# Kernel tuning notes

Measured on AMD Instinct MI355X. Metric: run time of the kernel, lower is better.

Reference implementation:

```python
import jax, jax.numpy as jnp
import numpy as np

B, NPG, DEG = 512, 128, 16          # graphs, nodes/graph, out-degree
N = B * NPG                          # 65536 nodes
E = N * DEG                          # 1048576 edges
IN_DIM, HID, HEADS = 11, 32, 4
K1 = int(np.ceil(0.8 * NPG))         # 103 nodes/graph after pool1
K2 = int(np.ceil(0.8 * K1))          # 83 nodes/graph after pool2


def gat_conv(x, src, dst, mask, W, a_s, a_d, b, n_nodes):
    # PyG GATConv (concat=True, add_self_loops=True, eval mode -> no dropout)
    xp = (x @ W).reshape(n_nodes, HEADS, HID)            # [N,H,C]
    as_ = jnp.einsum('nhc,hc->nh', xp, a_s)
    ad_ = jnp.einsum('nhc,hc->nh', xp, a_d)
    loop = jnp.arange(n_nodes)
    s = jnp.concatenate([src, loop])
    d = jnp.concatenate([dst, loop])
    m = jnp.concatenate([mask, jnp.ones(n_nodes, bool)])
    logit = jax.nn.leaky_relu(as_[s] + ad_[d], 0.2)      # [E+N,H]
    logit = jnp.where(m[:, None], logit, -1e9)
    mx = jax.ops.segment_max(logit, d, num_segments=n_nodes)
    ex = jnp.exp(logit - mx[d]) * m[:, None]
    den = jax.ops.segment_sum(ex, d, num_segments=n_nodes)
    alpha = ex / (den[d] + 1e-16)                        # segment softmax over dst
    out = jax.ops.segment_sum(alpha[:, :, None] * xp[s], d, num_segments=n_nodes)
    return out.reshape(n_nodes, HEADS * HID) + b


def topk_pool(x, src, dst, mask, w, npg, k):
    # PyG TopKPooling: score = tanh((x*w).sum(-1)/||w||); keep top ceil(ratio*n) per graph
    nb = x.shape[0] // npg
    score = jnp.tanh((x @ w) / jnp.linalg.norm(w))
    vals, idx = jax.lax.top_k(score.reshape(nb, npg), k)  # [B,k]
    perm = (idx + (jnp.arange(nb) * npg)[:, None]).reshape(-1)
    x_new = x[perm] * vals.reshape(-1, 1)
    remap = jnp.full(nb * npg, -1).at[perm].set(jnp.arange(nb * k))
    ns, nd = remap[src], remap[dst]
    m = mask & (ns >= 0) & (nd >= 0)
    return x_new, jnp.where(m, ns, 0), jnp.where(m, nd, 0), m


def setup_inputs():
    key = jax.random.key(0)
    ks = jax.random.split(key, 24)
    s = 0.05
    x = jax.random.normal(ks[0], (N, IN_DIM), jnp.float32)
    src = jnp.repeat(jnp.arange(N), DEG)
    dst = (src // NPG) * NPG + jax.random.randint(ks[1], (E,), 0, NPG)
    edge_index = jnp.stack([src, dst])
    edge_attr = jax.random.normal(ks[2], (E, 4), jnp.float32)
    batch = jnp.repeat(jnp.arange(B), NPG)
    p = dict(
        W_g1=jax.random.normal(ks[3], (IN_DIM, HEADS * HID), jnp.float32) * s,
        att_src1=jax.random.normal(ks[4], (HEADS, HID), jnp.float32) * s,
        att_dst1=jax.random.normal(ks[5], (HEADS, HID), jnp.float32) * s,
        b_g1=jnp.zeros((HEADS * HID,), jnp.float32),
        W_t1=jax.random.normal(ks[6], (HEADS * HID, HID), jnp.float32) * s,
        b_t1=jnp.zeros((HID,), jnp.float32),
        pool_w1=jax.random.normal(ks[7], (HID,), jnp.float32) * s,
        W_g2=jax.random.normal(ks[8], (HID, HEADS * HID), jnp.float32) * s,
        att_src2=jax.random.normal(ks[9], (HEADS, HID), jnp.float32) * s,
        att_dst2=jax.random.normal(ks[10], (HEADS, HID), jnp.float32) * s,
        b_g2=jnp.zeros((HEADS * HID,), jnp.float32),
        W_t2=jax.random.normal(ks[11], (HEADS * HID, HID), jnp.float32) * s,
        b_t2=jnp.zeros((HID,), jnp.float32),
        pool_w2=jax.random.normal(ks[12], (HID,), jnp.float32) * s,
        W_l1=jax.random.normal(ks[13], (2 * HID, 256), jnp.float32) * s,
        b_l1=jnp.zeros((256,), jnp.float32),
        W_l2=jax.random.normal(ks[14], (256, 1024), jnp.float32) * s,
        b_l2=jnp.zeros((1024,), jnp.float32),
        W_l3=jax.random.normal(ks[15], (1024, 1), jnp.float32) * s,
        b_l3=jnp.zeros((1,), jnp.float32),
    )
    return dict(x=x, edge_index=edge_index, edge_attr=edge_attr, batch=batch, **p)


def reference(x, edge_index, edge_attr, batch,
              W_g1, att_src1, att_dst1, b_g1, W_t1, b_t1, pool_w1,
              W_g2, att_src2, att_dst2, b_g2, W_t2, b_t2, pool_w2,
              W_l1, b_l1, W_l2, b_l2, W_l3, b_l3):
    # edge_attr is ignored (GATConv built without edge_dim); batch is implicit
    # in the fixed equal-size graph layout.  Eval mode -> dropout disabled.
    src, dst = edge_index[0], edge_index[1]
    mask = jnp.ones(E, bool)
    h = jax.nn.relu(gat_conv(x, src, dst, mask, W_g1, att_src1, att_dst1, b_g1, N))
    h = h @ W_t1 + b_t1
    h, src, dst, mask = topk_pool(h, src, dst, mask, pool_w1, NPG, K1)
    h1 = h.reshape(B, K1, HID)
    g1 = jnp.concatenate([h1.max(1), h1.mean(1)], axis=1)   # [B, 2*HID]
    h = jax.nn.relu(gat_conv(h, src, dst, mask, W_g2, att_src2, att_dst2, b_g2, B * K1))
    h = h @ W_t2 + b_t2
    h, src, dst, mask = topk_pool(h, src, dst, mask, pool_w2, K1, K2)
    h2 = h.reshape(B, K2, HID)
    g2 = jnp.concatenate([h2.max(1), h2.mean(1)], axis=1)
    g = g1 + g2
    g = jax.nn.relu(g @ W_l1 + b_l1)
    g = jax.nn.relu(g @ W_l2 + b_l2)
    return g @ W_l3 + b_l3                                   # [B,1]
```

## Files before the change

kernel.cpp:

```cpp
#include <hip/hip_runtime.h>
#include <math.h>

constexpr int NPGc  = 128;
constexpr int NG    = 512;
constexpr int EPGc  = 2048;
constexpr int ETOT  = 1048576;
constexpr int IND   = 11;
constexpr int HIDc  = 32;
constexpr int FD    = 128;
constexpr int K1c   = 103;
constexpr int K2c   = 83;
constexpr int NN    = NG * NPGc;
constexpr int N2c   = NG * K1c;

__device__ __forceinline__ float lrelu(float x){ return fmaxf(x, 0.2f*x); }

__device__ __forceinline__ unsigned flipF(float f){
    unsigned u = __float_as_uint(f);
    return u ^ (unsigned)(((int)u >> 31) | 0x80000000);
}
__device__ __forceinline__ float unflipF(unsigned u){
    unsigned m = ((u >> 31) - 1u) | 0x80000000u;
    return __uint_as_float(u ^ m);
}

template<int KIN>
__device__ void foldDev(const float* __restrict__ Wg, const float* __restrict__ avs,
                        const float* __restrict__ avd, float* __restrict__ S, float* __restrict__ D, int t)
{
    if (t < KIN * 4) {
        int k = t >> 2, h = t & 3;
        float s = 0.f, d = 0.f;
        for (int j = 0; j < HIDc; j++) {
            float w = Wg[k*FD + h*HIDc + j];
            s = fmaf(w, avs[h*HIDc + j], s);
            d = fmaf(w, avd[h*HIDc + j], d);
        }
        S[t] = s; D[t] = d;
    }
}

__global__ __launch_bounds__(256) void k_prep(const int* __restrict__ ei,
    const float* __restrict__ W1g, const float* __restrict__ s1, const float* __restrict__ d1,
    const float* __restrict__ W2g, const float* __restrict__ s2, const float* __restrict__ d2,
    int* __restrict__ csrOff, unsigned char* __restrict__ csrSB, unsigned char* __restrict__ csrDB,
    float* __restrict__ S1, float* __restrict__ D1, float* __restrict__ S2, float* __restrict__ D2)
{
    int b = blockIdx.x, t = threadIdx.x;
    if (b >= NG) {
        if (b == NG)     foldDev<IND>(W1g, s1, d1, S1, D1, t);
        else             foldDev<HIDc>(W2g, s2, d2, S2, D2, t);
        return;
    }
    int g = b;
    __shared__ int cnt[128], cur[128], offL[129];
    __shared__ unsigned char sbL[EPGc], dbL[EPGc];
    if (t < 128) cnt[t] = 0;
    __syncthreads();
    const int* dstG = ei + ETOT + g * EPGc;
    int dnv[8];
    #pragma unroll
    for (int q = 0; q < 8; q++) {
        int e = t + 256*q;
        dnv[q] = dstG[e] - g * NPGc;
        atomicAdd(&cnt[dnv[q]], 1);
    }
    __syncthreads();
    if (t < 64) {
        int c0 = cnt[2*t], c1 = cnt[2*t + 1], ps = c0 + c1, P = ps;
        #pragma unroll
        for (int dl = 1; dl < 64; dl <<= 1) { int v = __shfl_up(P, dl); if (t >= dl) P += v; }
        int E0 = P - ps;
        offL[2*t] = E0; offL[2*t + 1] = E0 + c0;
        cur[2*t]  = E0; cur[2*t + 1]  = E0 + c0;
        if (t == 63) offL[128] = P;
    }
    __syncthreads();
    #pragma unroll
    for (int q = 0; q < 8; q++) {
        int e = t + 256*q;
        int pos = atomicAdd(&cur[dnv[q]], 1);
        sbL[pos] = (unsigned char)(e >> 4);
        dbL[pos] = (unsigned char)dnv[q];
    }
    __syncthreads();
    if (t < 128) {
        ((int4*)(csrSB + (size_t)g * EPGc))[t] = ((const int4*)sbL)[t];
        ((int4*)(csrDB + (size_t)g * EPGc))[t] = ((const int4*)dbL)[t];
    }
    if (t <= NPGc) csrOff[g*132 + t] = offL[t];
}

template<int NNODE, int KIN, int KEEP, bool FIRST>
__global__ __launch_bounds__(256, 4) void k_layer(
    const float* __restrict__ xin, const float* __restrict__ Wg,
    const float* __restrict__ WsS, const float* __restrict__ WsD,
    const float* __restrict__ bg,
    const float* __restrict__ Wt, const float* __restrict__ bt,
    const float* __restrict__ pw,
    const int* __restrict__ csrOff, const unsigned char* __restrict__ csrSB,
    const unsigned char* __restrict__ csrDB,
    const int* __restrict__ ei,
    int* __restrict__ csrOffW, unsigned char* __restrict__ sbW,
    unsigned char* __restrict__ dbW,
    float* __restrict__ xnew,
    float* __restrict__ gfeat, const float* __restrict__ gprev,
    const float* __restrict__ W1, const float* __restrict__ b1,
    const float* __restrict__ W2, const float* __restrict__ b2,
    const float* __restrict__ W3, const float* __restrict__ b3,
    float* __restrict__ outp)
{
    constexpr int NP   = (NNODE + 3) & ~3;
    constexpr int NGRP = NP / 4;
    int g = blockIdx.x, t = threadIdx.x;

    __shared__ __align__(16) float xFT[KIN * NP];
    __shared__ __align__(16) float WgsL[KIN * 32];
    __shared__ __align__(16) float WtsL[1024];
    __shared__ __align__(16) float xpL[NP * 36];
    __shared__ float wEu[EPGc];
    __shared__ unsigned char sbL[EPGc], dbL[EPGc];
    __shared__ int offL[NNODE + 1 > 129 ? NNODE + 1 : 129];
    __shared__ float asL[NNODE], adL[NNODE], sfW[NNODE], sDi[NNODE];
    __shared__ unsigned maxU[NNODE];
    __shared__ float WsSL[KIN * 4], WsDL[KIN * 4], bgL[FD], btL[HIDc];
    __shared__ float gvec[64];
    float* mLn = (float*)maxU;

    {
        const float* xg = xin + (size_t)g * NNODE * KIN;
        for (int i = t; i < NNODE * KIN; i += 256) {
            int n = i / KIN, k = i - n * KIN;
            xFT[k * NP + n] = xg[i];
        }
        if constexpr (NP > NNODE) {
            for (int i = t; i < KIN * (NP - NNODE); i += 256) {
                int k = i / (NP - NNODE), n = NNODE + (i % (NP - NNODE));
                xFT[k * NP + n] = 0.f;
            }
        }
    }
    for (int i = t; i < KIN * 4; i += 256) { WsSL[i] = WsS[i]; WsDL[i] = WsD[i]; }
    if (t < FD) bgL[t] = bg[t];
    if (t < HIDc) btL[t] = bt[t];
    if (t <= NNODE) offL[t] = csrOff[g*132 + t];
    for (int i = t; i < EPGc / 16; i += 256) {
        ((int4*)sbL)[i] = ((const int4*)(csrSB + (size_t)g * EPGc))[i];
        ((int4*)dbL)[i] = ((const int4*)(csrDB + (size_t)g * EPGc))[i];
    }
    __syncthreads();
    const int EC = offL[NNODE];

    const int n4 = t >> 3, j4 = t & 7;
    float4 acc0, acc1, acc2, acc3;
    { float4 bi = make_float4(btL[j4*4], btL[j4*4+1], btL[j4*4+2], btL[j4*4+3]);
      acc0 = bi; acc1 = bi; acc2 = bi; acc3 = bi; }

    for (int h = 0; h < 4; h++) {
        __syncthreads();

        for (int i = t; i < KIN * 32; i += 256) WgsL[i] = Wg[(i >> 5)*FD + h*32 + (i & 31)];
        ((float4*)WtsL)[t] = ((const float4*)(Wt + h*1024))[t];
        __syncthreads();

        for (int id = t; id < NGRP * 32; id += 256) {
            int grp = id >> 5, c = id & 31;
            float4 a = make_float4(0.f, 0.f, 0.f, 0.f);
            #pragma unroll
            for (int k = 0; k < KIN; k++) {
                float4 xv = *(const float4*)&xFT[k * NP + grp * 4];
                float w = WgsL[k*32 + c];
                a.x = fmaf(xv.x, w, a.x); a.y = fmaf(xv.y, w, a.y);
                a.z = fmaf(xv.z, w, a.z); a.w = fmaf(xv.w, w, a.w);
            }
            int nb = grp * 4;
            xpL[(nb+0)*36 + c] = a.x; xpL[(nb+1)*36 + c] = a.y;
            xpL[(nb+2)*36 + c] = a.z; xpL[(nb+3)*36 + c] = a.w;
        }
        if (t < NNODE) {
            float s = 0.f, d = 0.f;
            #pragma unroll
            for (int k = 0; k < KIN; k++) {
                float v = xFT[k * NP + t];
                s = fmaf(v, WsSL[k*4 + h], s);
                d = fmaf(v, WsDL[k*4 + h], d);
            }
            asL[t] = s; adL[t] = d; maxU[t] = flipF(s);
        }
        __syncthreads();

        for (int s = t; s < EC; s += 256)
            atomicMax(&maxU[dbL[s]], flipF(asL[sbL[s]]));
        __syncthreads();

        if (t < NNODE) {
            float ad = adL[t];
            float m = lrelu(unflipF(maxU[t]) + ad);
            sfW[t] = expf(lrelu(asL[t] + ad) - m);
            mLn[t] = m;
        }
        __syncthreads();

        for (int s = t; s < EC; s += 256) {
            int sb = sbL[s], db = dbL[s];
            wEu[s] = expf(lrelu(asL[sb] + adL[db]) - mLn[db]);
        }
        __syncthreads();

        if (t < NNODE) {
            float den = sfW[t];
            int lo = offL[t], hi = offL[t + 1];
            for (int s = lo; s < hi; s++) den += wEu[s];
            sDi[t] = 1.f / (den + 1e-16f);
        }
        __syncthreads();

        const float4* X4 = (const float4*)xpL;
        auto aggOne = [&](int p) -> float4 {
            int n = p >> 3, c4 = p & 7;
            float w0 = sfW[n];
            float4 v = X4[n*9 + c4];
            float4 a; a.x = w0*v.x; a.y = w0*v.y; a.z = w0*v.z; a.w = w0*v.w;
            int lo = offL[n], hi = offL[n + 1];
            for (int s = lo; s < hi; s++) {
                int sc = sbL[s]; float w = wEu[s];
                float4 u = X4[sc*9 + c4];
                a.x = fmaf(w, u.x, a.x); a.y = fmaf(w, u.y, a.y);
                a.z = fmaf(w, u.z, a.z); a.w = fmaf(w, u.w, a.w);
            }
            float inv = sDi[n];
            float4 r;
            r.x = fmaxf(fmaf(a.x, inv, bgL[h*32 + c4*4 + 0]), 0.f);
            r.y = fmaxf(fmaf(a.y, inv, bgL[h*32 + c4*4 + 1]), 0.f);
            r.z = fmaxf(fmaf(a.z, inv, bgL[h*32 + c4*4 + 2]), 0.f);
            r.w = fmaxf(fmaf(a.w, inv, bgL[h*32 + c4*4 + 3]), 0.f);
            return r;
        };
        float4 rv0 = aggOne(t);
        float4 rv1 = aggOne(t + 256);
        float4 rv2 = aggOne(t + 512);
        float4 rv3;
        if (t + 768 < NNODE * 8) rv3 = aggOne(t + 768);
        __syncthreads();

        float4* X4w = (float4*)xpL;
        X4w[(t>>3)*9 + (t&7)] = rv0;
        { int p = t + 256; X4w[(p>>3)*9 + (p&7)] = rv1; }
        { int p = t + 512; X4w[(p>>3)*9 + (p&7)] = rv2; }
        if (t + 768 < NNODE * 8) { int p = t + 768; X4w[(p>>3)*9 + (p&7)] = rv3; }
        __syncthreads();

        if (n4 < NGRP) {
            int nb = n4 * 4;
            #pragma unroll 8
            for (int c = 0; c < 32; c++) {
                float4 w4 = *(const float4*)&WtsL[c*HIDc + j4*4];
                float r0 = xpL[(nb+0)*36 + c], r1 = xpL[(nb+1)*36 + c];
                float r2 = xpL[(nb+2)*36 + c], r3 = xpL[(nb+3)*36 + c];
                acc0.x = fmaf(r0, w4.x, acc0.x); acc0.y = fmaf(r0, w4.y, acc0.y);
                acc0.z = fmaf(r0, w4.z, acc0.z); acc0.w = fmaf(r0, w4.w, acc0.w);
                acc1.x = fmaf(r1, w4.x, acc1.x); acc1.y = fmaf(r1, w4.y, acc1.y);
                acc1.z = fmaf(r1, w4.z, acc1.z); acc1.w = fmaf(r1, w4.w, acc1.w);
                acc2.x = fmaf(r2, w4.x, acc2.x); acc2.y = fmaf(r2, w4.y, acc2.y);
                acc2.z = fmaf(r2, w4.z, acc2.z); acc2.w = fmaf(r2, w4.w, acc2.w);
                acc3.x = fmaf(r3, w4.x, acc3.x); acc3.y = fmaf(r3, w4.y, acc3.y);
                acc3.z = fmaf(r3, w4.z, acc3.z); acc3.w = fmaf(r3, w4.w, acc3.w);
            }
        }
    }
    __syncthreads();

    float* htL = xpL;
    if (n4 < NGRP) {
        int nb = n4 * 4, jb = j4 * 4;
        float4 av[4] = {acc0, acc1, acc2, acc3};
        #pragma unroll
        for (int i = 0; i < 4; i++) {
            int n = nb + i;
            if (n < NNODE) {
                htL[n*33 + jb + 0] = av[i].x; htL[n*33 + jb + 1] = av[i].y;
                htL[n*33 + jb + 2] = av[i].z; htL[n*33 + jb + 3] = av[i].w;
            }
        }
    }
    __syncthreads();

    float* scoreL = wEu;
    int*   rnkL   = (int*)(wEu + 128);
    float nrm; { float ss = 0.f; for (int k = 0; k < HIDc; k++) { float w = pw[k]; ss = fmaf(w, w, ss); } nrm = sqrtf(ss); }
    if (t < NNODE) {
        float dot = 0.f;
        for (int k = 0; k < HIDc; k++) dot = fmaf(htL[t*33 + k], pw[k], dot);
        scoreL[t] = tanhf(dot / nrm);
    }
    __syncthreads();
    if (t < NNODE) {
        float si = scoreL[t]; int rank = 0;
        for (int q = 0; q < NNODE; q++) {
            float sj = scoreL[q];
            rank += (sj > si || (sj == si && q < t)) ? 1 : 0;
        }
        rnkL[t] = (rank < KEEP) ? rank : -1;
    }
    __syncthreads();
    if constexpr (FIRST) {
        for (int p = t; p < NNODE * 32; p += 256) {
            int n = p >> 5, jj = p & 31;
            int rk = rnkL[n];
            if (rk >= 0) xnew[((size_t)g*KEEP + rk)*HIDc + jj] = htL[n*33 + jj] * scoreL[n];
        }
    }
    if (t < HIDc) {
        float mx = -INFINITY, sm = 0.f;
        for (int n = 0; n < NNODE; n++) {
            if (rnkL[n] >= 0) { float v = htL[n*33 + t] * scoreL[n]; mx = fmaxf(mx, v); sm += v; }
        }
        float mean = sm / (float)KEEP;
        if constexpr (FIRST) {
            gfeat[(size_t)g*64 + t]      = mx;
            gfeat[(size_t)g*64 + 32 + t] = mean;
        } else {
            gvec[t]      = gprev[(size_t)g*64 + t] + mx;
            gvec[32 + t] = gprev[(size_t)g*64 + 32 + t] + mean;
        }
    }

    if constexpr (FIRST) {
        __syncthreads();
        int* cnt = (int*)maxU;
        int* cur = (int*)sfW;
        if (t < 128) cnt[t] = 0;
        __syncthreads();
        const int* dstG = ei + ETOT + g * EPGc;
        int snv[8], dnv[8];
        #pragma unroll
        for (int q = 0; q < 8; q++) {
            int e = t + 256*q;
            int s = rnkL[e >> 4], d = rnkL[dstG[e] - g * NPGc];
            bool ok = (s >= 0 && d >= 0);
            snv[q] = s; dnv[q] = ok ? d : -1;
            if (ok) atomicAdd(&cnt[d], 1);
        }
        __syncthreads();
        if (t < 64) {
            int c0 = cnt[2*t], c1 = cnt[2*t + 1], ps = c0 + c1, P = ps;
            #pragma unroll
            for (int dl = 1; dl < 64; dl <<= 1) { int v = __shfl_up(P, dl); if (t >= dl) P += v; }
            int E0 = P - ps;
            offL[2*t] = E0; offL[2*t + 1] = E0 + c0;
            cur[2*t]  = E0; cur[2*t + 1]  = E0 + c0;
            if (t == 63) offL[128] = P;
        }
        __syncthreads();
        #pragma unroll
        for (int q = 0; q < 8; q++) {
            if (dnv[q] >= 0) {
                int pos = atomicAdd(&cur[dnv[q]], 1);
                sbL[pos] = (unsigned char)snv[q];
                dbL[pos] = (unsigned char)dnv[q];
            }
        }
        __syncthreads();
        if (t < 128) {
            ((int4*)(sbW + (size_t)g * EPGc))[t] = ((const int4*)sbL)[t];
            ((int4*)(dbW + (size_t)g * EPGc))[t] = ((const int4*)dbL)[t];
        }
        if (t <= K1c) csrOffW[g*132 + t] = offL[t];
    } else {
        __syncthreads();
        float* h1L = wEu;
        float* red = wEu + 256;
        float a = b1[t];
        #pragma unroll 4
        for (int k = 0; k < 64; k++) a = fmaf(gvec[k], W1[k*256 + t], a);
        h1L[t] = fmaxf(a, 0.f);
        __syncthreads();
        float c0 = b2[t], c1 = b2[t + 256], c2 = b2[t + 512], c3 = b2[t + 768];
        const float* w2c = W2 + t;
        #pragma unroll 4
        for (int i = 0; i < 256; i++) {
            float hv = h1L[i];
            const float* wr = w2c + (size_t)i * 1024;
            c0 = fmaf(hv, wr[0],   c0);
            c1 = fmaf(hv, wr[256], c1);
            c2 = fmaf(hv, wr[512], c2);
            c3 = fmaf(hv, wr[768], c3);
        }
        float p = fmaf(fmaxf(c0, 0.f), W3[t],
                  fmaf(fmaxf(c1, 0.f), W3[t + 256],
                  fmaf(fmaxf(c2, 0.f), W3[t + 512],
                       fmaxf(c3, 0.f) * W3[t + 768])));
        red[t] = p;
        __syncthreads();
        for (int s = 128; s > 0; s >>= 1) { if (t < s) red[t] += red[t + s]; __syncthreads(); }
        if (t == 0) outp[g] = red[0] + b3[0];
    }
}

extern "C" void kernel_launch(void* const* d_in, const int* in_sizes, int n_in,
                              void* d_out, int out_size, void* d_ws, size_t ws_size,
                              hipStream_t stream)
{
    const float* x    = (const float*)d_in[0];
    const int*   ei   = (const int*)  d_in[1];
    const float* W_g1 = (const float*)d_in[4];
    const float* as1w = (const float*)d_in[5];
    const float* ad1w = (const float*)d_in[6];
    const float* b_g1 = (const float*)d_in[7];
    const float* W_t1 = (const float*)d_in[8];
    const float* b_t1 = (const float*)d_in[9];
    const float* pw1  = (const float*)d_in[10];
    const float* W_g2 = (const float*)d_in[11];
    const float* as2w = (const float*)d_in[12];
    const float* ad2w = (const float*)d_in[13];
    const float* b_g2 = (const float*)d_in[14];
    const float* W_t2 = (const float*)d_in[15];
    const float* b_t2 = (const float*)d_in[16];
    const float* pw2  = (const float*)d_in[17];
    const float* W_l1 = (const float*)d_in[18];
    const float* b_l1 = (const float*)d_in[19];
    const float* W_l2 = (const float*)d_in[20];
    const float* b_l2 = (const float*)d_in[21];
    const float* W_l3 = (const float*)d_in[22];
    const float* b_l3 = (const float*)d_in[23];
    float* out = (float*)d_out;

    char* ws = (char*)d_ws;
    size_t off = 0;
    auto alloc = [&](size_t bytes) -> void* {
        void* p = (void*)(ws + off);
        off += ((bytes + 255) / 256) * 256;
        return p;
    };
    float* x2    = (float*)alloc((size_t)N2c * HIDc * 4);
    float* g1    = (float*)alloc((size_t)NG * 64 * 4);
    float* wsS1  = (float*)alloc(64 * 4);
    float* wsD1  = (float*)alloc(64 * 4);
    float* wsS2  = (float*)alloc(128 * 4);
    float* wsD2  = (float*)alloc(128 * 4);
    int*   off1  = (int*)  alloc((size_t)NG * 132 * 4);
    unsigned char* sb1 = (unsigned char*)alloc((size_t)NG * EPGc);
    unsigned char* db1 = (unsigned char*)alloc((size_t)NG * EPGc);
    int*   off2  = (int*)  alloc((size_t)NG * 132 * 4);
    unsigned char* sb2 = (unsigned char*)alloc((size_t)NG * EPGc);
    unsigned char* db2 = (unsigned char*)alloc((size_t)NG * EPGc);

    k_prep<<<NG + 2, 256, 0, stream>>>(ei, W_g1, as1w, ad1w, W_g2, as2w, ad2w,
                                       off1, sb1, db1, wsS1, wsD1, wsS2, wsD2);

    k_layer<NPGc, IND, K1c, true><<<NG, 256, 0, stream>>>(
        x, W_g1, wsS1, wsD1, b_g1, W_t1, b_t1, pw1,
        off1, sb1, db1,
        ei, off2, sb2, db2,
        x2, g1, nullptr,
        nullptr, nullptr, nullptr, nullptr, nullptr, nullptr, nullptr);

    k_layer<K1c, HIDc, K2c, false><<<NG, 256, 0, stream>>>(
        x2, W_g2, wsS2, wsD2, b_g2, W_t2, b_t2, pw2,
        off2, sb2, db2,
        nullptr, nullptr, nullptr, nullptr,
        nullptr, nullptr, g1,
        W_l1, b_l1, W_l2, b_l2, W_l3, b_l3, out);
}
```

Baseline: 318.8 us.

## Split GAT layer into per-head kernels with separate linear+pool reduction kernel

Each fused per-graph layer kernel is split in two. A GAT kernel launched over a (graph, head) grid computes one head's projection, segment softmax and aggregation, then a partial transform by W_t into a global buffer. A linpool kernel sums the four head partials, adds the bias and runs top-k pooling, CSR rebuild and the final MLP. The atomic-max pass and the stored dst-byte array are replaced by a per-destination CSR loop that computes max, exponentials and denominator in one thread. This raises parallelism fourfold, and in exchange adds two launches and a large global round-trip for the per-head partials.

```diff
diff --git a/kernel.cpp b/kernel.cpp
--- a/kernel.cpp
+++ b/kernel.cpp
@@ -15,15 +15,6 @@
 
 __device__ __forceinline__ float lrelu(float x){ return fmaxf(x, 0.2f*x); }
 
-__device__ __forceinline__ unsigned flipF(float f){
-    unsigned u = __float_as_uint(f);
-    return u ^ (unsigned)(((int)u >> 31) | 0x80000000);
-}
-__device__ __forceinline__ float unflipF(unsigned u){
-    unsigned m = ((u >> 31) - 1u) | 0x80000000u;
-    return __uint_as_float(u ^ m);
-}
-
 template<int KIN>
 __device__ void foldDev(const float* __restrict__ Wg, const float* __restrict__ avs,
                         const float* __restrict__ avd, float* __restrict__ S, float* __restrict__ D, int t)
@@ -43,7 +34,7 @@
 __global__ __launch_bounds__(256) void k_prep(const int* __restrict__ ei,
     const float* __restrict__ W1g, const float* __restrict__ s1, const float* __restrict__ d1,
     const float* __restrict__ W2g, const float* __restrict__ s2, const float* __restrict__ d2,
-    int* __restrict__ csrOff, unsigned char* __restrict__ csrSB, unsigned char* __restrict__ csrDB,
+    int* __restrict__ csrOff, unsigned char* __restrict__ csrSB,
     float* __restrict__ S1, float* __restrict__ D1, float* __restrict__ S2, float* __restrict__ D2)
 {
     int b = blockIdx.x, t = threadIdx.x;
@@ -54,7 +45,7 @@
     }
     int g = b;
     __shared__ int cnt[128], cur[128], offL[129];
-    __shared__ unsigned char sbL[EPGc], dbL[EPGc];
+    __shared__ unsigned char sbL[EPGc];
     if (t < 128) cnt[t] = 0;
     __syncthreads();
     const int* dstG = ei + ETOT + g * EPGc;
@@ -81,222 +72,196 @@
         int e = t + 256*q;
         int pos = atomicAdd(&cur[dnv[q]], 1);
         sbL[pos] = (unsigned char)(e >> 4);
-        dbL[pos] = (unsigned char)dnv[q];
-    }
-    __syncthreads();
-    if (t < 128) {
-        ((int4*)(csrSB + (size_t)g * EPGc))[t] = ((const int4*)sbL)[t];
-        ((int4*)(csrDB + (size_t)g * EPGc))[t] = ((const int4*)dbL)[t];
-    }
+    }
+    __syncthreads();
+    if (t < 128) ((int4*)(csrSB + (size_t)g * EPGc))[t] = ((const int4*)sbL)[t];
     if (t <= NPGc) csrOff[g*132 + t] = offL[t];
 }
 
-template<int NNODE, int KIN, int KEEP, bool FIRST>
-__global__ __launch_bounds__(256, 4) void k_layer(
+template<int NNODE, int KIN>
+__global__ __launch_bounds__(256) void k_gat(
     const float* __restrict__ xin, const float* __restrict__ Wg,
     const float* __restrict__ WsS, const float* __restrict__ WsD,
-    const float* __restrict__ bg,
-    const float* __restrict__ Wt, const float* __restrict__ bt,
-    const float* __restrict__ pw,
     const int* __restrict__ csrOff, const unsigned char* __restrict__ csrSB,
-    const unsigned char* __restrict__ csrDB,
-    const int* __restrict__ ei,
+    const float* __restrict__ bias, const float* __restrict__ Wt,
+    float* __restrict__ htp)
+{
+    int g = blockIdx.x, h = blockIdx.y, t = threadIdx.x;
+    constexpr int UN = (NNODE*KIN > EPGc ? NNODE*KIN : EPGc);
+    __shared__ __align__(16) float xpL[NNODE * 36];
+    __shared__ __align__(16) float uni[UN];
+    __shared__ __align__(16) unsigned char sbL[EPGc];
+    __shared__ float asL[NNODE], adL[NNODE], sfW[NNODE], sDen[NNODE];
+    __shared__ int offL[NNODE + 1];
+    __shared__ float WL[KIN * 32];
+    __shared__ float WsSL[KIN], WsDL[KIN], bL[32];
+    __shared__ __align__(16) float WtsL[1024];
+
+    float* xF  = uni;
+    float* wEL = uni;
+
+    {
+        const float* xg = xin + (size_t)g * NNODE * KIN;
+        if constexpr ((KIN & 3) == 0) {
+            for (int i = t; i < NNODE * (KIN/4); i += 256)
+                ((float4*)xF)[i] = ((const float4*)xg)[i];
+        } else {
+            for (int i = t; i < NNODE * KIN; i += 256) xF[i] = xg[i];
+        }
+    }
+    for (int i = t; i < KIN * 32; i += 256) { int k = i >> 5, c = i & 31; WL[i] = Wg[k*FD + h*32 + c]; }
+    if (t < KIN) { WsSL[t] = WsS[t*4 + h]; WsDL[t] = WsD[t*4 + h]; }
+    if (t < 32) bL[t] = bias[h*32 + t];
+    if (t <= NNODE) offL[t] = csrOff[g*132 + t];
+    if (t < 128) ((int4*)sbL)[t] = ((const int4*)(csrSB + (size_t)g * EPGc))[t];
+    ((float4*)WtsL)[t] = ((const float4*)(Wt + h*1024))[t];
+    __syncthreads();
+
+    for (int p = t; p < NNODE * 32; p += 256) {
+        int n = p >> 5, c = p & 31;
+        const float* xr = xF + n * KIN;
+        float acc = 0.f;
+        #pragma unroll
+        for (int k = 0; k < KIN; k++) acc = fmaf(xr[k], WL[k*32 + c], acc);
+        xpL[n*36 + c] = acc;
+    }
+    if (t < NNODE) {
+        const float* xr = xF + t * KIN;
+        float s = 0.f, d = 0.f;
+        #pragma unroll
+        for (int k = 0; k < KIN; k++) { float v = xr[k]; s = fmaf(v, WsSL[k], s); d = fmaf(v, WsDL[k], d); }
+        asL[t] = s; adL[t] = d;
+    }
+    __syncthreads();
+
+    if (t < NNODE) {
+        float as_n = asL[t], adn = adL[t];
+        int lo = offL[t], hi = offL[t + 1];
+        float mx = as_n;
+        for (int i = lo; i < hi; i++) mx = fmaxf(mx, asL[sbL[i]]);
+        float m = lrelu(mx + adn);
+        float ws = expf(lrelu(as_n + adn) - m);
+        float den = ws;
+        for (int i = lo; i < hi; i++) {
+            float w = expf(lrelu(asL[sbL[i]] + adn) - m);
+            wEL[i] = w; den += w;
+        }
+        sfW[t] = ws; sDen[t] = den;
+    }
+    __syncthreads();
+
+    const float4* X4 = (const float4*)xpL;
+    float4 rv[4];
+    #pragma unroll
+    for (int r = 0; r < 4; r++) {
+        int p = t + r*256;
+        if (p < NNODE * 8) {
+            int n = p >> 3, c4 = p & 7;
+            float w0 = sfW[n];
+            float4 v = X4[n*9 + c4];
+            float4 a; a.x = w0*v.x; a.y = w0*v.y; a.z = w0*v.z; a.w = w0*v.w;
+            int lo = offL[n], hi = offL[n + 1];
+            for (int s = lo; s < hi; s++) {
+                int sc = sbL[s]; float w = wEL[s];
+                float4 u = X4[sc*9 + c4];
+                a.x = fmaf(w, u.x, a.x); a.y = fmaf(w, u.y, a.y);
+                a.z = fmaf(w, u.z, a.z); a.w = fmaf(w, u.w, a.w);
+            }
+            float inv = 1.f / (sDen[n] + 1e-16f);
+            rv[r].x = fmaxf(fmaf(a.x, inv, bL[c4*4 + 0]), 0.f);
+            rv[r].y = fmaxf(fmaf(a.y, inv, bL[c4*4 + 1]), 0.f);
+            rv[r].z = fmaxf(fmaf(a.z, inv, bL[c4*4 + 2]), 0.f);
+            rv[r].w = fmaxf(fmaf(a.w, inv, bL[c4*4 + 3]), 0.f);
+        }
+    }
+    __syncthreads();
+    {
+        float4* X4w = (float4*)xpL;
+        #pragma unroll
+        for (int r = 0; r < 4; r++) {
+            int p = t + r*256;
+            if (p < NNODE * 8) X4w[(p>>3)*9 + (p&7)] = rv[r];
+        }
+    }
+    __syncthreads();
+
+    const int n0 = t >> 3, j4 = t & 7;
+    float4 a0 = make_float4(0,0,0,0), a1 = a0, a2 = a0, a3 = a0;
+    #pragma unroll 8
+    for (int c = 0; c < 32; c++) {
+        float4 w4 = *(const float4*)&WtsL[c*HIDc + j4*4];
+        float r0 = xpL[n0*36 + c];
+        a0.x = fmaf(r0, w4.x, a0.x); a0.y = fmaf(r0, w4.y, a0.y);
+        a0.z = fmaf(r0, w4.z, a0.z); a0.w = fmaf(r0, w4.w, a0.w);
+        if (n0 + 32 < NNODE) {
+            float r1 = xpL[(n0+32)*36 + c];
+            a1.x = fmaf(r1, w4.x, a1.x); a1.y = fmaf(r1, w4.y, a1.y);
+            a1.z = fmaf(r1, w4.z, a1.z); a1.w = fmaf(r1, w4.w, a1.w);
+        }
+        if (n0 + 64 < NNODE) {
+            float r2 = xpL[(n0+64)*36 + c];
+            a2.x = fmaf(r2, w4.x, a2.x); a2.y = fmaf(r2, w4.y, a2.y);
+            a2.z = fmaf(r2, w4.z, a2.z); a2.w = fmaf(r2, w4.w, a2.w);
+        }
+        if (n0 + 96 < NNODE) {
+            float r3 = xpL[(n0+96)*36 + c];
+            a3.x = fmaf(r3, w4.x, a3.x); a3.y = fmaf(r3, w4.y, a3.y);
+            a3.z = fmaf(r3, w4.z, a3.z); a3.w = fmaf(r3, w4.w, a3.w);
+        }
+    }
+    {
+        size_t base = ((size_t)(g * NNODE + n0) * 4 + h) * 32 + j4 * 4;
+        *(float4*)(htp + base) = a0;
+        if (n0 + 32 < NNODE) *(float4*)(htp + base + (size_t)32*128) = a1;
+        if (n0 + 64 < NNODE) *(float4*)(htp + base + (size_t)64*128) = a2;
+        if (n0 + 96 < NNODE) *(float4*)(htp + base + (size_t)96*128) = a3;
+    }
+}
+
+template<int NIN, int KEEP, bool FIRST>
+__global__ __launch_bounds__(256) void k_linpool(
+    const float* __restrict__ htp, const float* __restrict__ bt, const float* __restrict__ pw,
+    float* __restrict__ xnew, const int* __restrict__ ei,
     int* __restrict__ csrOffW, unsigned char* __restrict__ sbW,
-    unsigned char* __restrict__ dbW,
-    float* __restrict__ xnew,
     float* __restrict__ gfeat, const float* __restrict__ gprev,
     const float* __restrict__ W1, const float* __restrict__ b1,
     const float* __restrict__ W2, const float* __restrict__ b2,
     const float* __restrict__ W3, const float* __restrict__ b3,
     float* __restrict__ outp)
 {
-    constexpr int NP   = (NNODE + 3) & ~3;
-    constexpr int NGRP = NP / 4;
     int g = blockIdx.x, t = threadIdx.x;
-
-    __shared__ __align__(16) float xFT[KIN * NP];
-    __shared__ __align__(16) float WgsL[KIN * 32];
-    __shared__ __align__(16) float WtsL[1024];
-    __shared__ __align__(16) float xpL[NP * 36];
-    __shared__ float wEu[EPGc];
-    __shared__ unsigned char sbL[EPGc], dbL[EPGc];
-    __shared__ int offL[NNODE + 1 > 129 ? NNODE + 1 : 129];
-    __shared__ float asL[NNODE], adL[NNODE], sfW[NNODE], sDi[NNODE];
-    __shared__ unsigned maxU[NNODE];
-    __shared__ float WsSL[KIN * 4], WsDL[KIN * 4], bgL[FD], btL[HIDc];
+    __shared__ float htL[NIN * 33];
+    __shared__ float scoreL[NIN];
+    __shared__ int rnkL[NIN];
+    __shared__ int cnt[128], cur[128], offL[129];
+    __shared__ unsigned char sbL[EPGc];
     __shared__ float gvec[64];
-    float* mLn = (float*)maxU;
-
-    {
-        const float* xg = xin + (size_t)g * NNODE * KIN;
-        for (int i = t; i < NNODE * KIN; i += 256) {
-            int n = i / KIN, k = i - n * KIN;
-            xFT[k * NP + n] = xg[i];
-        }
-        if constexpr (NP > NNODE) {
-            for (int i = t; i < KIN * (NP - NNODE); i += 256) {
-                int k = i / (NP - NNODE), n = NNODE + (i % (NP - NNODE));
-                xFT[k * NP + n] = 0.f;
-            }
-        }
-    }
-    for (int i = t; i < KIN * 4; i += 256) { WsSL[i] = WsS[i]; WsDL[i] = WsD[i]; }
-    if (t < FD) bgL[t] = bg[t];
-    if (t < HIDc) btL[t] = bt[t];
-    if (t <= NNODE) offL[t] = csrOff[g*132 + t];
-    for (int i = t; i < EPGc / 16; i += 256) {
-        ((int4*)sbL)[i] = ((const int4*)(csrSB + (size_t)g * EPGc))[i];
-        ((int4*)dbL)[i] = ((const int4*)(csrDB + (size_t)g * EPGc))[i];
-    }
-    __syncthreads();
-    const int EC = offL[NNODE];
-
-    const int n4 = t >> 3, j4 = t & 7;
-    float4 acc0, acc1, acc2, acc3;
-    { float4 bi = make_float4(btL[j4*4], btL[j4*4+1], btL[j4*4+2], btL[j4*4+3]);
-      acc0 = bi; acc1 = bi; acc2 = bi; acc3 = bi; }
-
-    for (int h = 0; h < 4; h++) {
-        __syncthreads();
-
-        for (int i = t; i < KIN * 32; i += 256) WgsL[i] = Wg[(i >> 5)*FD + h*32 + (i & 31)];
-        ((float4*)WtsL)[t] = ((const float4*)(Wt + h*1024))[t];
-        __syncthreads();
-
-        for (int id = t; id < NGRP * 32; id += 256) {
-            int grp = id >> 5, c = id & 31;
-            float4 a = make_float4(0.f, 0.f, 0.f, 0.f);
-            #pragma unroll
-            for (int k = 0; k < KIN; k++) {
-                float4 xv = *(const float4*)&xFT[k * NP + grp * 4];
-                float w = WgsL[k*32 + c];
-                a.x = fmaf(xv.x, w, a.x); a.y = fmaf(xv.y, w, a.y);
-                a.z = fmaf(xv.z, w, a.z); a.w = fmaf(xv.w, w, a.w);
-            }
-            int nb = grp * 4;
-            xpL[(nb+0)*36 + c] = a.x; xpL[(nb+1)*36 + c] = a.y;
-            xpL[(nb+2)*36 + c] = a.z; xpL[(nb+3)*36 + c] = a.w;
-        }
-        if (t < NNODE) {
-            float s = 0.f, d = 0.f;
-            #pragma unroll
-            for (int k = 0; k < KIN; k++) {
-                float v = xFT[k * NP + t];
-                s = fmaf(v, WsSL[k*4 + h], s);
-                d = fmaf(v, WsDL[k*4 + h], d);
-            }
-            asL[t] = s; adL[t] = d; maxU[t] = flipF(s);
-        }
-        __syncthreads();
-
-        for (int s = t; s < EC; s += 256)
-            atomicMax(&maxU[dbL[s]], flipF(asL[sbL[s]]));
-        __syncthreads();
-
-        if (t < NNODE) {
-            float ad = adL[t];
-            float m = lrelu(unflipF(maxU[t]) + ad);
-            sfW[t] = expf(lrelu(asL[t] + ad) - m);
-            mLn[t] = m;
-        }
-        __syncthreads();
-
-        for (int s = t; s < EC; s += 256) {
-            int sb = sbL[s], db = dbL[s];
-            wEu[s] = expf(lrelu(asL[sb] + adL[db]) - mLn[db]);
-        }
-        __syncthreads();
-
-        if (t < NNODE) {
-            float den = sfW[t];
-            int lo = offL[t], hi = offL[t + 1];
-            for (int s = lo; s < hi; s++) den += wEu[s];
-            sDi[t] = 1.f / (den + 1e-16f);
-        }
-        __syncthreads();
-
-        const float4* X4 = (const float4*)xpL;
-        auto aggOne = [&](int p) -> float4 {
-            int n = p >> 3, c4 = p & 7;
-            float w0 = sfW[n];
-            float4 v = X4[n*9 + c4];
-            float4 a; a.x = w0*v.x; a.y = w0*v.y; a.z = w0*v.z; a.w = w0*v.w;
-            int lo = offL[n], hi = offL[n + 1];
-            for (int s = lo; s < hi; s++) {
-                int sc = sbL[s]; float w = wEu[s];
-                float4 u = X4[sc*9 + c4];
-                a.x = fmaf(w, u.x, a.x); a.y = fmaf(w, u.y, a.y);
-                a.z = fmaf(w, u.z, a.z); a.w = fmaf(w, u.w, a.w);
-            }
-            float inv = sDi[n];
-            float4 r;
-            r.x = fmaxf(fmaf(a.x, inv, bgL[h*32 + c4*4 + 0]), 0.f);
-            r.y = fmaxf(fmaf(a.y, inv, bgL[h*32 + c4*4 + 1]), 0.f);
-            r.z = fmaxf(fmaf(a.z, inv, bgL[h*32 + c4*4 + 2]), 0.f);
-            r.w = fmaxf(fmaf(a.w, inv, bgL[h*32 + c4*4 + 3]), 0.f);
-            return r;
-        };
-        float4 rv0 = aggOne(t);
-        float4 rv1 = aggOne(t + 256);
-        float4 rv2 = aggOne(t + 512);
-        float4 rv3;
-        if (t + 768 < NNODE * 8) rv3 = aggOne(t + 768);
-        __syncthreads();
-
-        float4* X4w = (float4*)xpL;
-        X4w[(t>>3)*9 + (t&7)] = rv0;
-        { int p = t + 256; X4w[(p>>3)*9 + (p&7)] = rv1; }
-        { int p = t + 512; X4w[(p>>3)*9 + (p&7)] = rv2; }
-        if (t + 768 < NNODE * 8) { int p = t + 768; X4w[(p>>3)*9 + (p&7)] = rv3; }
-        __syncthreads();
-
-        if (n4 < NGRP) {
-            int nb = n4 * 4;
-            #pragma unroll 8
-            for (int c = 0; c < 32; c++) {
-                float4 w4 = *(const float4*)&WtsL[c*HIDc + j4*4];
-                float r0 = xpL[(nb+0)*36 + c], r1 = xpL[(nb+1)*36 + c];
-                float r2 = xpL[(nb+2)*36 + c], r3 = xpL[(nb+3)*36 + c];
-                acc0.x = fmaf(r0, w4.x, acc0.x); acc0.y = fmaf(r0, w4.y, acc0.y);
-                acc0.z = fmaf(r0, w4.z, acc0.z); acc0.w = fmaf(r0, w4.w, acc0.w);
-                acc1.x = fmaf(r1, w4.x, acc1.x); acc1.y = fmaf(r1, w4.y, acc1.y);
-                acc1.z = fmaf(r1, w4.z, acc1.z); acc1.w = fmaf(r1, w4.w, acc1.w);
-                acc2.x = fmaf(r2, w4.x, acc2.x); acc2.y = fmaf(r2, w4.y, acc2.y);
-                acc2.z = fmaf(r2, w4.z, acc2.z); acc2.w = fmaf(r2, w4.w, acc2.w);
-                acc3.x = fmaf(r3, w4.x, acc3.x); acc3.y = fmaf(r3, w4.y, acc3.y);
-                acc3.z = fmaf(r3, w4.z, acc3.z); acc3.w = fmaf(r3, w4.w, acc3.w);
-            }
-        }
-    }
-    __syncthreads();
-
-    float* htL = xpL;
-    if (n4 < NGRP) {
-        int nb = n4 * 4, jb = j4 * 4;
-        float4 av[4] = {acc0, acc1, acc2, acc3};
-        #pragma unroll
-        for (int i = 0; i < 4; i++) {
-            int n = nb + i;
-            if (n < NNODE) {
-                htL[n*33 + jb + 0] = av[i].x; htL[n*33 + jb + 1] = av[i].y;
-                htL[n*33 + jb + 2] = av[i].z; htL[n*33 + jb + 3] = av[i].w;
-            }
-        }
-    }
-    __syncthreads();
-
-    float* scoreL = wEu;
-    int*   rnkL   = (int*)(wEu + 128);
+    __shared__ float h1L[256], red[256];
+
+    for (int p = t; p < NIN * 8; p += 256) {
+        int n = p >> 3, q = p & 7;
+        const float4* row = (const float4*)(htp + (size_t)(g * NIN + n) * 128);
+        float4 s = ((const float4*)bt)[q];
+        float4 p0 = row[q], p1 = row[8 + q], p2 = row[16 + q], p3 = row[24 + q];
+        s.x += p0.x; s.y += p0.y; s.z += p0.z; s.w += p0.w;
+        s.x += p1.x; s.y += p1.y; s.z += p1.z; s.w += p1.w;
+        s.x += p2.x; s.y += p2.y; s.z += p2.z; s.w += p2.w;
+        s.x += p3.x; s.y += p3.y; s.z += p3.z; s.w += p3.w;
+        float* d = htL + n*33 + q*4;
+        d[0] = s.x; d[1] = s.y; d[2] = s.z; d[3] = s.w;
+    }
+    __syncthreads();
+
     float nrm; { float ss = 0.f; for (int k = 0; k < HIDc; k++) { float w = pw[k]; ss = fmaf(w, w, ss); } nrm = sqrtf(ss); }
-    if (t < NNODE) {
+    if (t < NIN) {
         float dot = 0.f;
         for (int k = 0; k < HIDc; k++) dot = fmaf(htL[t*33 + k], pw[k], dot);
         scoreL[t] = tanhf(dot / nrm);
     }
     __syncthreads();
-    if (t < NNODE) {
+    if (t < NIN) {
         float si = scoreL[t]; int rank = 0;
-        for (int q = 0; q < NNODE; q++) {
+        for (int q = 0; q < NIN; q++) {
             float sj = scoreL[q];
             rank += (sj > si || (sj == si && q < t)) ? 1 : 0;
         }
@@ -304,7 +269,7 @@
     }
     __syncthreads();
     if constexpr (FIRST) {
-        for (int p = t; p < NNODE * 32; p += 256) {
+        for (int p = t; p < NIN * 32; p += 256) {
             int n = p >> 5, jj = p & 31;
             int rk = rnkL[n];
             if (rk >= 0) xnew[((size_t)g*KEEP + rk)*HIDc + jj] = htL[n*33 + jj] * scoreL[n];
@@ -312,7 +277,7 @@
     }
     if (t < HIDc) {
         float mx = -INFINITY, sm = 0.f;
-        for (int n = 0; n < NNODE; n++) {
+        for (int n = 0; n < NIN; n++) {
             if (rnkL[n] >= 0) { float v = htL[n*33 + t] * scoreL[n]; mx = fmaxf(mx, v); sm += v; }
         }
         float mean = sm / (float)KEEP;
@@ -327,8 +292,6 @@
 
     if constexpr (FIRST) {
         __syncthreads();
-        int* cnt = (int*)maxU;
-        int* cur = (int*)sfW;
         if (t < 128) cnt[t] = 0;
         __syncthreads();
         const int* dstG = ei + ETOT + g * EPGc;
@@ -357,19 +320,13 @@
             if (dnv[q] >= 0) {
                 int pos = atomicAdd(&cur[dnv[q]], 1);
                 sbL[pos] = (unsigned char)snv[q];
-                dbL[pos] = (unsigned char)dnv[q];
             }
         }
         __syncthreads();
-        if (t < 128) {
-            ((int4*)(sbW + (size_t)g * EPGc))[t] = ((const int4*)sbL)[t];
-            ((int4*)(dbW + (size_t)g * EPGc))[t] = ((const int4*)dbL)[t];
-        }
+        if (t < 128) ((int4*)(sbW + (size_t)g * EPGc))[t] = ((const int4*)sbL)[t];
         if (t <= K1c) csrOffW[g*132 + t] = offL[t];
     } else {
         __syncthreads();
-        float* h1L = wEu;
-        float* red = wEu + 256;
         float a = b1[t];
         #pragma unroll 4
         for (int k = 0; k < 64; k++) a = fmaf(gvec[k], W1[k*256 + t], a);
@@ -432,6 +389,8 @@
         off += ((bytes + 255) / 256) * 256;
         return p;
     };
+    float* htp1  = (float*)alloc((size_t)NN * 128 * 4);
+    float* htp2  = (float*)alloc((size_t)N2c * 128 * 4);
     float* x2    = (float*)alloc((size_t)N2c * HIDc * 4);
     float* g1    = (float*)alloc((size_t)NG * 64 * 4);
     float* wsS1  = (float*)alloc(64 * 4);
@@ -440,25 +399,23 @@
     float* wsD2  = (float*)alloc(128 * 4);
     int*   off1  = (int*)  alloc((size_t)NG * 132 * 4);
     unsigned char* sb1 = (unsigned char*)alloc((size_t)NG * EPGc);
-    unsigned char* db1 = (unsigned char*)alloc((size_t)NG * EPGc);
     int*   off2  = (int*)  alloc((size_t)NG * 132 * 4);
     unsigned char* sb2 = (unsigned char*)alloc((size_t)NG * EPGc);
-    unsigned char* db2 = (unsigned char*)alloc((size_t)NG * EPGc);
 
     k_prep<<<NG + 2, 256, 0, stream>>>(ei, W_g1, as1w, ad1w, W_g2, as2w, ad2w,
-                                       off1, sb1, db1, wsS1, wsD1, wsS2, wsD2);
-
-    k_layer<NPGc, IND, K1c, true><<<NG, 256, 0, stream>>>(
-        x, W_g1, wsS1, wsD1, b_g1, W_t1, b_t1, pw1,
-        off1, sb1, db1,
-        ei, off2, sb2, db2,
-        x2, g1, nullptr,
+                                       off1, sb1, wsS1, wsD1, wsS2, wsD2);
+
+    k_gat<NPGc, IND><<<dim3(NG, 4), 256, 0, stream>>>(
+        x, W_g1, wsS1, wsD1, off1, sb1, b_g1, W_t1, htp1);
+
+    k_linpool<NPGc, K1c, true><<<NG, 256, 0, stream>>>(
+        htp1, b_t1, pw1, x2, ei, off2, sb2, g1, nullptr,
         nullptr, nullptr, nullptr, nullptr, nullptr, nullptr, nullptr);
 
-    k_layer<K1c, HIDc, K2c, false><<<NG, 256, 0, stream>>>(
-        x2, W_g2, wsS2, wsD2, b_g2, W_t2, b_t2, pw2,
-        off2, sb2, db2,
-        nullptr, nullptr, nullptr, nullptr,
-        nullptr, nullptr, g1,
+    k_gat<K1c, HIDc><<<dim3(NG, 4), 256, 0, stream>>>(
+        x2, W_g2, wsS2, wsD2, off2, sb2, b_g2, W_t2, htp2);
+
+    k_linpool<K1c, K2c, false><<<NG, 256, 0, stream>>>(
+        htp2, b_t2, pw2, nullptr, nullptr, nullptr, nullptr, nullptr, g1,
         W_l1, b_l1, W_l2, b_l2, W_l3, b_l3, out);
 }
```

Measured after the change: 296.1 us. 7.1% less time.
